# Kernel optimization log

Hardware: AMD Instinct MI355X
Metric: run time of the kernel (lower is better)

Reference implementation:

```python
import jax, jax.numpy as jnp
import numpy as np

N = 16384          # number of vectors to quantize (flattened leading dims)
K = 2 ** 14        # codebook_size = 2**bits_per_codeword
D = 64             # vector_dim


def setup_inputs() -> dict:
    key = jax.random.key(0)
    k1, k2, k3, k4 = jax.random.split(key, 4)
    x_re = jax.random.normal(k1, (N, D), dtype=jnp.float32)
    x_im = jax.random.normal(k2, (N, D), dtype=jnp.float32)
    # random complex codebook, normalized so each row has unit complex L2 norm
    cb_re = jax.random.normal(k3, (K, D), dtype=jnp.float32)
    cb_im = jax.random.normal(k4, (K, D), dtype=jnp.float32)
    norm = jnp.sqrt(jnp.sum(cb_re * cb_re + cb_im * cb_im, axis=1, keepdims=True))
    cb_re = cb_re / norm
    cb_im = cb_im / norm
    return {"x_re": x_re, "x_im": x_im, "cb_re": cb_re, "cb_im": cb_im}


def reference(x_re, x_im, cb_re, cb_im):
    # complex inner product conj(x) . c, expanded in real arithmetic:
    #   Re = x_re.c_re + x_im.c_im ;  Im = x_re.c_im - x_im.c_re
    dot_re = jnp.einsum('nd,kd->nk', x_re, cb_re) + jnp.einsum('nd,kd->nk', x_im, cb_im)
    dot_im = jnp.einsum('nd,kd->nk', x_re, cb_im) - jnp.einsum('nd,kd->nk', x_im, cb_re)
    mag = jnp.sqrt(dot_re * dot_re + dot_im * dot_im)  # [N, K] abs of complex dot
    indices = jnp.argmax(mag, axis=-1)                 # [N] int
    # reconstruction: gather codebook rows (call() with int input)
    recon = jnp.stack([cb_re[indices], cb_im[indices]], axis=-1)  # [N, D, 2] (re, im)
    return indices, recon
```

## Files before the change

kernel.cpp:

```cpp
#include <hip/hip_runtime.h>

#define NROWS 16384
#define KCB   16384
#define DD    64
#define BM    256
#define CSPLIT 16
#define COLS_PER_BLOCK 1024
#define TILE_COLS 128
#define NTILES (COLS_PER_BLOCK / TILE_COLS)
#define NCHUNK (TILE_COLS / 16)
#define CAP 2048
#define DELTA 0.45f
#define TILE_BYTES 32768

typedef __attribute__((ext_vector_type(8))) short bf16x8;
typedef __attribute__((ext_vector_type(4))) float f32x4;

__device__ __forceinline__ unsigned pk_bf16(float lo, float hi) {
    unsigned a = __float_as_uint(lo);
    unsigned b = __float_as_uint(hi);
    a += 0x7FFFu + ((a >> 16) & 1u);
    b += 0x7FFFu + ((b >> 16) & 1u);
    return (a >> 16) | (b & 0xFFFF0000u);
}

__device__ __forceinline__ bf16x8 mk8(unsigned a, unsigned b, unsigned c, unsigned d) {
    union { uint4 u; bf16x8 v; } x;
    x.u = make_uint4(a, b, c, d);
    return x.v;
}

__device__ __forceinline__ unsigned swz(unsigned row, unsigned byte_in_row) {
    return row * 128u + (byte_in_row ^ ((row & 7u) << 4));
}

__device__ __forceinline__ void gload_lds16(const void* g, void* l) {
    __builtin_amdgcn_global_load_lds(
        (__attribute__((address_space(1))) void*)(g),
        (__attribute__((address_space(3))) void*)(l), 16, 0, 0);
}

__global__ __launch_bounds__(256) void prep(
    const float* __restrict__ cb_re, const float* __restrict__ cb_im,
    uint4* __restrict__ cb_sw,
    unsigned* __restrict__ row_max_bits, unsigned long long* __restrict__ best_packed,
    int do_conv)
{
    int id = blockIdx.x * 256 + threadIdx.x;
    if (id < NROWS) { row_max_bits[id] = 0u; best_packed[id] = 0ull; }
    if (!do_conv) return;
    int u   = id & 1023;
    int arr = (id >> 10) & 1;
    int gt  = id >> 11;
    int c   = u >> 3;
    int b   = ((u & 7) * 16) ^ ((c & 7) << 4);
    int col = gt * TILE_COLS + c;
    int d0  = b >> 1;
    const float* src = arr ? cb_im : cb_re;
    const float4* p = (const float4*)(src + (size_t)col * DD + d0);
    float4 f0 = p[0], f1 = p[1];
    cb_sw[id] = make_uint4(pk_bf16(f0.x, f0.y), pk_bf16(f0.z, f0.w),
                           pk_bf16(f1.x, f1.y), pk_bf16(f1.z, f1.w));
}

template<int PASS, bool PRE>
__global__ __launch_bounds__(512, 2) void score_kernel(
    const float* __restrict__ x_re, const float* __restrict__ x_im,
    const float* __restrict__ cb_re, const float* __restrict__ cb_im,
    const char* __restrict__ cb_sw,
    unsigned* __restrict__ row_max_bits,
    unsigned long long* __restrict__ best_packed)
{
    __shared__ char Bls[2][2][TILE_COLS * 128];
    __shared__ unsigned cand[CAP];
    __shared__ int cand_cnt;

    const int tid  = threadIdx.x;
    const int lane = tid & 63;
    const int wid  = tid >> 6;
    const int row0 = blockIdx.x * BM;
    const int col0 = blockIdx.y * COLS_PER_BLOCK;
    const int l15  = lane & 15;
    const int lhi  = lane >> 4;

    if (tid == 0) cand_cnt = 0;

    bf16x8 Ar[2][2], Ai[2][2];
#pragma unroll
    for (int a = 0; a < 2; ++a) {
        const int row = row0 + wid * 32 + a * 16 + l15;
        {
            const float4* pr = (const float4*)(x_re + (size_t)row * DD + lhi * 8);
            const float4* pi = (const float4*)(x_im + (size_t)row * DD + lhi * 8);
            float4 r0 = pr[0], r1 = pr[1];
            float4 i0 = pi[0], i1 = pi[1];
            Ar[a][0] = mk8(pk_bf16(r0.x, r0.y), pk_bf16(r0.z, r0.w),
                           pk_bf16(r1.x, r1.y), pk_bf16(r1.z, r1.w));
            Ai[a][0] = mk8(pk_bf16(i0.x, i0.y), pk_bf16(i0.z, i0.w),
                           pk_bf16(i1.x, i1.y), pk_bf16(i1.z, i1.w));
        }
        {
            const float4* pr = (const float4*)(x_re + (size_t)row * DD + 32 + lhi * 8);
            const float4* pi = (const float4*)(x_im + (size_t)row * DD + 32 + lhi * 8);
            float4 r0 = pr[0], r1 = pr[1];
            float4 i0 = pi[0], i1 = pi[1];
            Ar[a][1] = mk8(pk_bf16(r0.x, r0.y), pk_bf16(r0.z, r0.w),
                           pk_bf16(r1.x, r1.y), pk_bf16(r1.z, r1.w));
            Ai[a][1] = mk8(pk_bf16(i0.x, i0.y), pk_bf16(i0.z, i0.w),
                           pk_bf16(i1.x, i1.y), pk_bf16(i1.z, i1.w));
        }
    }

    float rm[2][4];
    float thr[2][4];
#pragma unroll
    for (int a = 0; a < 2; ++a)
#pragma unroll
        for (int r = 0; r < 4; ++r) rm[a][r] = 0.0f;
    if (PASS == 2) {
#pragma unroll
        for (int a = 0; a < 2; ++a)
#pragma unroll
            for (int r = 0; r < 4; ++r) {
                int n = row0 + wid * 32 + a * 16 + lhi * 4 + r;
                float mx = __uint_as_float(row_max_bits[n]);
                float tm = sqrtf(mx) - DELTA;
                thr[a][r] = (tm > 0.0f) ? tm * tm : -1.0f;
            }
    }

#define CHUNK_BODY(T_IDX, CH)                                                   \
    {                                                                           \
        const char* B0 = &Bls[(T_IDX) & 1][0][0];                               \
        const char* B1 = &Bls[(T_IDX) & 1][1][0];                               \
        const int colLocal = (CH) * 16 + l15;                                   \
        unsigned off0 = swz(colLocal, lhi * 16);                                \
        unsigned off1 = swz(colLocal, 64 + lhi * 16);                           \
        bf16x8 br0 = *(const bf16x8*)(B0 + off0);                               \
        bf16x8 bi0 = *(const bf16x8*)(B1 + off0);                               \
        bf16x8 br1 = *(const bf16x8*)(B0 + off1);                               \
        bf16x8 bi1 = *(const bf16x8*)(B1 + off1);                               \
        f32x4 accre[2], accim[2];                                               \
        _Pragma("unroll")                                                       \
        for (int a = 0; a < 2; ++a) {                                           \
            accre[a] = (f32x4){0.f, 0.f, 0.f, 0.f};                             \
            accim[a] = (f32x4){0.f, 0.f, 0.f, 0.f};                             \
        }                                                                       \
        _Pragma("unroll")                                                       \
        for (int a = 0; a < 2; ++a) {                                           \
            accre[a] = __builtin_amdgcn_mfma_f32_16x16x32_bf16(Ar[a][0], br0, accre[a], 0, 0, 0); \
            accre[a] = __builtin_amdgcn_mfma_f32_16x16x32_bf16(Ai[a][0], bi0, accre[a], 0, 0, 0); \
            accre[a] = __builtin_amdgcn_mfma_f32_16x16x32_bf16(Ar[a][1], br1, accre[a], 0, 0, 0); \
            accre[a] = __builtin_amdgcn_mfma_f32_16x16x32_bf16(Ai[a][1], bi1, accre[a], 0, 0, 0); \
            accim[a] = __builtin_amdgcn_mfma_f32_16x16x32_bf16(Ar[a][0], bi0, accim[a], 0, 0, 0); \
            accim[a] = __builtin_amdgcn_mfma_f32_16x16x32_bf16(Ar[a][1], bi1, accim[a], 0, 0, 0); \
        }                                                                       \
        br0 = br0 ^ (short)0x8000;                                              \
        br1 = br1 ^ (short)0x8000;                                              \
        _Pragma("unroll")                                                       \
        for (int a = 0; a < 2; ++a) {                                           \
            accim[a] = __builtin_amdgcn_mfma_f32_16x16x32_bf16(Ai[a][0], br0, accim[a], 0, 0, 0); \
            accim[a] = __builtin_amdgcn_mfma_f32_16x16x32_bf16(Ai[a][1], br1, accim[a], 0, 0, 0); \
        }                                                                       \
        _Pragma("unroll")                                                       \
        for (int a = 0; a < 2; ++a)                                             \
            _Pragma("unroll")                                                   \
            for (int r = 0; r < 4; ++r) {                                       \
                float re = accre[a][r], im = accim[a][r];                       \
                float m2 = fmaf(re, re, im * im);                               \
                if (PASS == 1) {                                                \
                    rm[a][r] = fmaxf(rm[a][r], m2);                             \
                } else {                                                        \
                    if (m2 >= thr[a][r]) {                                      \
                        int n = row0 + wid * 32 + a * 16 + lhi * 4 + r;         \
                        int k = col0 + (T_IDX) * TILE_COLS + (CH) * 16 + l15;   \
                        int idx = atomicAdd(&cand_cnt, 1);                      \
                        if (idx < CAP) cand[idx] = ((unsigned)n << 14) | (unsigned)k; \
                    }                                                           \
                }                                                               \
            }                                                                   \
    }

    if constexpr (PRE) {
        const char* tile_base = cb_sw + (size_t)blockIdx.y * NTILES * TILE_BYTES;
        auto stage = [&](int buf, int t) {
            const char* src = tile_base + (size_t)t * TILE_BYTES;
            char* dst = &Bls[buf][0][0];
#pragma unroll
            for (int j = 0; j < 4; ++j)
                gload_lds16(src + j * 8192 + tid * 16, dst + j * 8192 + tid * 16);
        };

        stage(0, 0);
        __syncthreads();

        for (int t = 0; t < NTILES; ++t) {
            const int cur = t & 1;
            if (t + 1 < NTILES) {
                stage(cur ^ 1, t + 1);
                asm volatile("s_waitcnt vmcnt(4)" ::: "memory");
            } else {
                asm volatile("s_waitcnt vmcnt(0)" ::: "memory");
            }
            __builtin_amdgcn_sched_barrier(0);
            __builtin_amdgcn_s_barrier();
            __builtin_amdgcn_sched_barrier(0);

            for (int ch = 0; ch < NCHUNK; ++ch)
                CHUNK_BODY(t, ch)

            __builtin_amdgcn_sched_barrier(0);
            __builtin_amdgcn_s_barrier();
        }
        __syncthreads();
    } else {
        const int scol  = tid >> 2;
        const int sboff = (tid & 3) * 32;
        uint4 g[4];
        auto stage_load = [&](int t) {
            const int col = col0 + t * TILE_COLS + scol;
            const int d0  = (tid & 3) * 16;
            const float4* pr = (const float4*)(cb_re + (size_t)col * DD + d0);
            const float4* pi = (const float4*)(cb_im + (size_t)col * DD + d0);
            float4 a0 = pr[0], a1 = pr[1], a2 = pr[2], a3 = pr[3];
            float4 b0 = pi[0], b1 = pi[1], b2 = pi[2], b3 = pi[3];
            g[0] = make_uint4(pk_bf16(a0.x,a0.y), pk_bf16(a0.z,a0.w), pk_bf16(a1.x,a1.y), pk_bf16(a1.z,a1.w));
            g[1] = make_uint4(pk_bf16(a2.x,a2.y), pk_bf16(a2.z,a2.w), pk_bf16(a3.x,a3.y), pk_bf16(a3.z,a3.w));
            g[2] = make_uint4(pk_bf16(b0.x,b0.y), pk_bf16(b0.z,b0.w), pk_bf16(b1.x,b1.y), pk_bf16(b1.z,b1.w));
            g[3] = make_uint4(pk_bf16(b2.x,b2.y), pk_bf16(b2.z,b2.w), pk_bf16(b3.x,b3.y), pk_bf16(b3.z,b3.w));
        };
        auto stage_write = [&](int buf) {
            unsigned o0 = swz(scol, sboff);
            unsigned o1 = swz(scol, sboff + 16);
            *(uint4*)(&Bls[buf][0][0] + o0) = g[0];
            *(uint4*)(&Bls[buf][0][0] + o1) = g[1];
            *(uint4*)(&Bls[buf][1][0] + o0) = g[2];
            *(uint4*)(&Bls[buf][1][0] + o1) = g[3];
        };
        stage_load(0);
        stage_write(0);
        __syncthreads();
        for (int t = 0; t < NTILES; ++t) {
            if (t + 1 < NTILES) stage_load(t + 1);
            for (int ch = 0; ch < NCHUNK; ++ch)
                CHUNK_BODY(t, ch)
            if (t + 1 < NTILES) {
                stage_write(1 - (t & 1));
                __syncthreads();
            }
        }
        __syncthreads();
    }
#undef CHUNK_BODY

    if (PASS == 1) {
#pragma unroll
        for (int m = 1; m < 16; m <<= 1)
#pragma unroll
            for (int a = 0; a < 2; ++a)
#pragma unroll
                for (int r = 0; r < 4; ++r)
                    rm[a][r] = fmaxf(rm[a][r], __shfl_xor(rm[a][r], m, 64));
        if (l15 == 0) {
#pragma unroll
            for (int a = 0; a < 2; ++a)
#pragma unroll
                for (int r = 0; r < 4; ++r) {
                    int n = row0 + wid * 32 + a * 16 + lhi * 4 + r;
                    atomicMax(&row_max_bits[n], __float_as_uint(rm[a][r]));
                }
        }
    } else {
        int cnt = cand_cnt < CAP ? cand_cnt : CAP;
        for (int i = tid; i < cnt; i += 512) {
            unsigned e = cand[i];
            int n = (int)(e >> 14);
            int k = (int)(e & 16383u);
            const float* xr = x_re + (size_t)n * DD;
            const float* xi = x_im + (size_t)n * DD;
            const float* cr = cb_re + (size_t)k * DD;
            const float* ci = cb_im + (size_t)k * DD;
            float accr = 0.0f, acci = 0.0f;
            for (int d = 0; d < DD; ++d) {
                float xrv = xr[d], xiv = xi[d], crv = cr[d], civ = ci[d];
                accr = fmaf(xrv, crv, accr);
                accr = fmaf(xiv, civ, accr);
                acci = fmaf(xrv, civ, acci);
                acci = fmaf(-xiv, crv, acci);
            }
            float m2 = accr * accr + acci * acci;
            unsigned long long key =
                ((unsigned long long)__float_as_uint(m2) << 32) | (unsigned)(~(unsigned)k);
            atomicMax(&best_packed[n], key);
        }
    }
}

__global__ __launch_bounds__(256) void finalize(
    const unsigned long long* __restrict__ best_packed,
    const float* __restrict__ cb_re, const float* __restrict__ cb_im,
    float* __restrict__ out)
{
    const int wave = threadIdx.x >> 6;
    const int lane = threadIdx.x & 63;
    const int n = blockIdx.x * 4 + wave;
    if (n >= NROWS) return;

    unsigned long long p = best_packed[n];
    unsigned k = ~(unsigned)(p & 0xFFFFFFFFull);

    if (lane == 0) out[n] = (float)k;

    float re = cb_re[(size_t)k * DD + lane];
    float im = cb_im[(size_t)k * DD + lane];
    float2* ro = reinterpret_cast<float2*>(out + NROWS);
    ro[(size_t)n * DD + lane] = make_float2(re, im);
}

extern "C" void kernel_launch(void* const* d_in, const int* in_sizes, int n_in,
                              void* d_out, int out_size, void* d_ws, size_t ws_size,
                              hipStream_t stream)
{
    const float* x_re  = (const float*)d_in[0];
    const float* x_im  = (const float*)d_in[1];
    const float* cb_re = (const float*)d_in[2];
    const float* cb_im = (const float*)d_in[3];
    float* out = (float*)d_out;

    const size_t CB_SW_BYTES = (size_t)(KCB / TILE_COLS) * TILE_BYTES;
    const size_t NEED = CB_SW_BYTES + NROWS * 4 + NROWS * 8;
    const bool pre = (ws_size >= NEED);

    const char* cb_sw = (const char*)d_ws;
    unsigned* row_max_bits;
    unsigned long long* best_packed;
    if (pre) {
        row_max_bits = (unsigned*)((char*)d_ws + CB_SW_BYTES);
        best_packed  = (unsigned long long*)((char*)d_ws + CB_SW_BYTES + NROWS * 4);
    } else {
        row_max_bits = (unsigned*)d_ws;
        best_packed  = (unsigned long long*)((char*)d_ws + NROWS * 4);
    }

    prep<<<pre ? 1024 : (NROWS / 256), 256, 0, stream>>>(
        cb_re, cb_im, (uint4*)d_ws, row_max_bits, best_packed, pre ? 1 : 0);

    dim3 grid(NROWS / BM, CSPLIT);
    if (pre) {
        score_kernel<1, true><<<grid, 512, 0, stream>>>(x_re, x_im, cb_re, cb_im,
            cb_sw, row_max_bits, best_packed);
        score_kernel<2, true><<<grid, 512, 0, stream>>>(x_re, x_im, cb_re, cb_im,
            cb_sw, row_max_bits, best_packed);
    } else {
        score_kernel<1, false><<<grid, 512, 0, stream>>>(x_re, x_im, cb_re, cb_im,
            cb_sw, row_max_bits, best_packed);
        score_kernel<2, false><<<grid, 512, 0, stream>>>(x_re, x_im, cb_re, cb_im,
            cb_sw, row_max_bits, best_packed);
    }

    finalize<<<NROWS / 4, 256, 0, stream>>>(best_packed, cb_re, cb_im, out);
}
```

Baseline: 268.7 us.

## Fuse two-pass max/candidate scoring into a single pass with block-local thresholds

Replaces the two score passes (global row max, then candidate emission) with one kernel. Each block tracks per-row maxima in shared memory, starts emitting candidates once the first two tiles have set a threshold, and re-scores tiles 0 and 1 at the end. The column split drops to 8 so each block sees 2048 columns, which gives a tighter local max. Shared-memory overflow now falls back to inline exact rescoring. This removes one full MFMA pass over the codebook. In exchange, block-local thresholds are looser than a global max, so more candidates may be produced, and the non-precomputed fallback path is removed.

Result: slower. 496.6 us (+84.8%).

```diff
diff --git a/kernel.cpp b/kernel.cpp
--- a/kernel.cpp
+++ b/kernel.cpp
@@ -4,12 +4,12 @@
 #define KCB   16384
 #define DD    64
 #define BM    256
-#define CSPLIT 16
-#define COLS_PER_BLOCK 1024
+#define CSPLIT 8
+#define COLS_PER_BLOCK 2048
 #define TILE_COLS 128
-#define NTILES (COLS_PER_BLOCK / TILE_COLS)
-#define NCHUNK (TILE_COLS / 16)
-#define CAP 2048
+#define NTILES 16
+#define NCHUNK 8
+#define CAP 3584
 #define DELTA 0.45f
 #define TILE_BYTES 32768
 
@@ -40,15 +40,42 @@
         (__attribute__((address_space(3))) void*)(l), 16, 0, 0);
 }
 
+__device__ __noinline__ void rescore_one(
+    int n, int k,
+    const float* __restrict__ x_re, const float* __restrict__ x_im,
+    const float* __restrict__ cb_re, const float* __restrict__ cb_im,
+    unsigned long long* __restrict__ best_packed)
+{
+    const float4* xr = (const float4*)(x_re + (size_t)n * DD);
+    const float4* xi = (const float4*)(x_im + (size_t)n * DD);
+    const float4* cr = (const float4*)(cb_re + (size_t)k * DD);
+    const float4* ci = (const float4*)(cb_im + (size_t)k * DD);
+    float accr = 0.0f, acci = 0.0f;
+#pragma unroll 4
+    for (int d4 = 0; d4 < 16; ++d4) {
+        float4 a = xr[d4], b = xi[d4], c = cr[d4], e = ci[d4];
+        accr = fmaf(a.x, c.x, accr); accr = fmaf(b.x, e.x, accr);
+        acci = fmaf(a.x, e.x, acci); acci = fmaf(-b.x, c.x, acci);
+        accr = fmaf(a.y, c.y, accr); accr = fmaf(b.y, e.y, accr);
+        acci = fmaf(a.y, e.y, acci); acci = fmaf(-b.y, c.y, acci);
+        accr = fmaf(a.z, c.z, accr); accr = fmaf(b.z, e.z, accr);
+        acci = fmaf(a.z, e.z, acci); acci = fmaf(-b.z, c.z, acci);
+        accr = fmaf(a.w, c.w, accr); accr = fmaf(b.w, e.w, accr);
+        acci = fmaf(a.w, e.w, acci); acci = fmaf(-b.w, c.w, acci);
+    }
+    float m2 = accr * accr + acci * acci;
+    unsigned long long key =
+        ((unsigned long long)__float_as_uint(m2) << 32) | (unsigned)(~(unsigned)k);
+    atomicMax(best_packed + n, key);
+}
+
 __global__ __launch_bounds__(256) void prep(
     const float* __restrict__ cb_re, const float* __restrict__ cb_im,
     uint4* __restrict__ cb_sw,
-    unsigned* __restrict__ row_max_bits, unsigned long long* __restrict__ best_packed,
-    int do_conv)
+    unsigned long long* __restrict__ best_packed)
 {
     int id = blockIdx.x * 256 + threadIdx.x;
-    if (id < NROWS) { row_max_bits[id] = 0u; best_packed[id] = 0ull; }
-    if (!do_conv) return;
+    if (id < NROWS) best_packed[id] = 0ull;
     int u   = id & 1023;
     int arr = (id >> 10) & 1;
     int gt  = id >> 11;
@@ -63,16 +90,15 @@
                            pk_bf16(f1.x, f1.y), pk_bf16(f1.z, f1.w));
 }
 
-template<int PASS, bool PRE>
 __global__ __launch_bounds__(512, 2) void score_kernel(
     const float* __restrict__ x_re, const float* __restrict__ x_im,
     const float* __restrict__ cb_re, const float* __restrict__ cb_im,
     const char* __restrict__ cb_sw,
-    unsigned* __restrict__ row_max_bits,
     unsigned long long* __restrict__ best_packed)
 {
     __shared__ char Bls[2][2][TILE_COLS * 128];
     __shared__ unsigned cand[CAP];
+    __shared__ unsigned smax[BM];
     __shared__ int cand_cnt;
 
     const int tid  = threadIdx.x;
@@ -84,6 +110,7 @@
     const int lhi  = lane >> 4;
 
     if (tid == 0) cand_cnt = 0;
+    if (tid < BM) smax[tid] = 0u;
 
     bf16x8 Ar[2][2], Ai[2][2];
 #pragma unroll
@@ -116,20 +143,18 @@
 #pragma unroll
     for (int a = 0; a < 2; ++a)
 #pragma unroll
-        for (int r = 0; r < 4; ++r) rm[a][r] = 0.0f;
-    if (PASS == 2) {
+        for (int r = 0; r < 4; ++r) { rm[a][r] = 0.0f; thr[a][r] = __builtin_inff(); }
+
+    const char* tile_base = cb_sw + (size_t)blockIdx.y * NTILES * TILE_BYTES;
+    auto stage = [&](int buf, int t) {
+        const char* src = tile_base + (size_t)t * TILE_BYTES;
+        char* dst = &Bls[buf][0][0];
 #pragma unroll
-        for (int a = 0; a < 2; ++a)
-#pragma unroll
-            for (int r = 0; r < 4; ++r) {
-                int n = row0 + wid * 32 + a * 16 + lhi * 4 + r;
-                float mx = __uint_as_float(row_max_bits[n]);
-                float tm = sqrtf(mx) - DELTA;
-                thr[a][r] = (tm > 0.0f) ? tm * tm : -1.0f;
-            }
-    }
-
-#define CHUNK_BODY(T_IDX, CH)                                                   \
+        for (int j = 0; j < 4; ++j)
+            gload_lds16(src + j * 8192 + tid * 16, dst + j * 8192 + tid * 16);
+    };
+
+#define CHUNK_BODY(T_IDX, CH, TRACK, EMIT)                                      \
     {                                                                           \
         const char* B0 = &Bls[(T_IDX) & 1][0][0];                               \
         const char* B1 = &Bls[(T_IDX) & 1][1][0];                               \
@@ -168,131 +193,101 @@
             for (int r = 0; r < 4; ++r) {                                       \
                 float re = accre[a][r], im = accim[a][r];                       \
                 float m2 = fmaf(re, re, im * im);                               \
-                if (PASS == 1) {                                                \
-                    rm[a][r] = fmaxf(rm[a][r], m2);                             \
-                } else {                                                        \
+                if (TRACK) rm[a][r] = fmaxf(rm[a][r], m2);                      \
+                if (EMIT) {                                                     \
                     if (m2 >= thr[a][r]) {                                      \
-                        int n = row0 + wid * 32 + a * 16 + lhi * 4 + r;         \
-                        int k = col0 + (T_IDX) * TILE_COLS + (CH) * 16 + l15;   \
+                        int nl = wid * 32 + a * 16 + lhi * 4 + r;               \
+                        int k  = col0 + (T_IDX) * TILE_COLS + (CH) * 16 + l15;  \
                         int idx = atomicAdd(&cand_cnt, 1);                      \
-                        if (idx < CAP) cand[idx] = ((unsigned)n << 14) | (unsigned)k; \
+                        if (idx < CAP) {                                        \
+                            cand[idx] = ((unsigned)nl << 14) | (unsigned)k;     \
+                        } else {                                                \
+                               \
+                            rescore_one(row0 + nl, k, x_re, x_im,               \
+                                        cb_re, cb_im, best_packed);             \
+                        }                                                       \
                     }                                                           \
                 }                                                               \
             }                                                                   \
     }
 
-    if constexpr (PRE) {
-        const char* tile_base = cb_sw + (size_t)blockIdx.y * NTILES * TILE_BYTES;
-        auto stage = [&](int buf, int t) {
-            const char* src = tile_base + (size_t)t * TILE_BYTES;
-            char* dst = &Bls[buf][0][0];
-#pragma unroll
-            for (int j = 0; j < 4; ++j)
-                gload_lds16(src + j * 8192 + tid * 16, dst + j * 8192 + tid * 16);
-        };
-
-        stage(0, 0);
-        __syncthreads();
-
-        for (int t = 0; t < NTILES; ++t) {
-            const int cur = t & 1;
-            if (t + 1 < NTILES) {
-                stage(cur ^ 1, t + 1);
-                asm volatile("s_waitcnt vmcnt(4)" ::: "memory");
-            } else {
-                asm volatile("s_waitcnt vmcnt(0)" ::: "memory");
-            }
-            __builtin_amdgcn_sched_barrier(0);
-            __builtin_amdgcn_s_barrier();
-            __builtin_amdgcn_sched_barrier(0);
-
+#define FOLD_SMAX()                                                             \
+    {                                                                           \
+        _Pragma("unroll")                                                       \
+        for (int m = 1; m < 16; m <<= 1)                                        \
+            _Pragma("unroll")                                                   \
+            for (int a = 0; a < 2; ++a)                                         \
+                _Pragma("unroll")                                               \
+                for (int r = 0; r < 4; ++r)                                     \
+                    rm[a][r] = fmaxf(rm[a][r], __shfl_xor(rm[a][r], m, 64));    \
+        if (l15 == 0) {                                                         \
+            _Pragma("unroll")                                                   \
+            for (int a = 0; a < 2; ++a)                                         \
+                _Pragma("unroll")                                               \
+                for (int r = 0; r < 4; ++r)                                     \
+                    atomicMax(&smax[wid * 32 + a * 16 + lhi * 4 + r],           \
+                              __float_as_uint(rm[a][r]));                       \
+        }                                                                       \
+    }
+
+#define LOAD_THR()                                                              \
+    {                                                                           \
+        _Pragma("unroll")                                                       \
+        for (int a = 0; a < 2; ++a)                                             \
+            _Pragma("unroll")                                                   \
+            for (int r = 0; r < 4; ++r) {                                       \
+                float mx = __uint_as_float(smax[wid * 32 + a * 16 + lhi * 4 + r]); \
+                float tm = sqrtf(mx) - DELTA;                                   \
+                thr[a][r] = (tm > 0.0f) ? tm * tm : -1.0f;                      \
+            }                                                                   \
+    }
+
+    stage(0, 0);
+    __syncthreads();
+
+    for (int t = 0; t < NTILES; ++t) {
+        stage((t + 1) & 1, (t + 1) & 15);
+        asm volatile("s_waitcnt vmcnt(4)" ::: "memory");
+        __builtin_amdgcn_sched_barrier(0);
+        __builtin_amdgcn_s_barrier();
+        __builtin_amdgcn_sched_barrier(0);
+
+        if (t >= 2) {
+            LOAD_THR()
             for (int ch = 0; ch < NCHUNK; ++ch)
-                CHUNK_BODY(t, ch)
-
-            __builtin_amdgcn_sched_barrier(0);
-            __builtin_amdgcn_s_barrier();
+                CHUNK_BODY(t, ch, 1, 1)
+        } else {
+            for (int ch = 0; ch < NCHUNK; ++ch)
+                CHUNK_BODY(t, ch, 1, 0)
         }
-        __syncthreads();
-    } else {
-        const int scol  = tid >> 2;
-        const int sboff = (tid & 3) * 32;
-        uint4 g[4];
-        auto stage_load = [&](int t) {
-            const int col = col0 + t * TILE_COLS + scol;
-            const int d0  = (tid & 3) * 16;
-            const float4* pr = (const float4*)(cb_re + (size_t)col * DD + d0);
-            const float4* pi = (const float4*)(cb_im + (size_t)col * DD + d0);
-            float4 a0 = pr[0], a1 = pr[1], a2 = pr[2], a3 = pr[3];
-            float4 b0 = pi[0], b1 = pi[1], b2 = pi[2], b3 = pi[3];
-            g[0] = make_uint4(pk_bf16(a0.x,a0.y), pk_bf16(a0.z,a0.w), pk_bf16(a1.x,a1.y), pk_bf16(a1.z,a1.w));
-            g[1] = make_uint4(pk_bf16(a2.x,a2.y), pk_bf16(a2.z,a2.w), pk_bf16(a3.x,a3.y), pk_bf16(a3.z,a3.w));
-            g[2] = make_uint4(pk_bf16(b0.x,b0.y), pk_bf16(b0.z,b0.w), pk_bf16(b1.x,b1.y), pk_bf16(b1.z,b1.w));
-            g[3] = make_uint4(pk_bf16(b2.x,b2.y), pk_bf16(b2.z,b2.w), pk_bf16(b3.x,b3.y), pk_bf16(b3.z,b3.w));
-        };
-        auto stage_write = [&](int buf) {
-            unsigned o0 = swz(scol, sboff);
-            unsigned o1 = swz(scol, sboff + 16);
-            *(uint4*)(&Bls[buf][0][0] + o0) = g[0];
-            *(uint4*)(&Bls[buf][0][0] + o1) = g[1];
-            *(uint4*)(&Bls[buf][1][0] + o0) = g[2];
-            *(uint4*)(&Bls[buf][1][0] + o1) = g[3];
-        };
-        stage_load(0);
-        stage_write(0);
-        __syncthreads();
-        for (int t = 0; t < NTILES; ++t) {
-            if (t + 1 < NTILES) stage_load(t + 1);
-            for (int ch = 0; ch < NCHUNK; ++ch)
-                CHUNK_BODY(t, ch)
-            if (t + 1 < NTILES) {
-                stage_write(1 - (t & 1));
-                __syncthreads();
-            }
-        }
-        __syncthreads();
-    }
+        FOLD_SMAX()
+
+        __builtin_amdgcn_sched_barrier(0);
+        __builtin_amdgcn_s_barrier();
+    }
+
+    stage(1, 1);
+    asm volatile("s_waitcnt vmcnt(0)" ::: "memory");
+    __builtin_amdgcn_sched_barrier(0);
+    __builtin_amdgcn_s_barrier();
+    __builtin_amdgcn_sched_barrier(0);
+    LOAD_THR()
+    for (int ch = 0; ch < NCHUNK; ++ch)
+        CHUNK_BODY(0, ch, 0, 1)
+    for (int ch = 0; ch < NCHUNK; ++ch)
+        CHUNK_BODY(1, ch, 0, 1)
+
+    __syncthreads();
+
 #undef CHUNK_BODY
-
-    if (PASS == 1) {
-#pragma unroll
-        for (int m = 1; m < 16; m <<= 1)
-#pragma unroll
-            for (int a = 0; a < 2; ++a)
-#pragma unroll
-                for (int r = 0; r < 4; ++r)
-                    rm[a][r] = fmaxf(rm[a][r], __shfl_xor(rm[a][r], m, 64));
-        if (l15 == 0) {
-#pragma unroll
-            for (int a = 0; a < 2; ++a)
-#pragma unroll
-                for (int r = 0; r < 4; ++r) {
-                    int n = row0 + wid * 32 + a * 16 + lhi * 4 + r;
-                    atomicMax(&row_max_bits[n], __float_as_uint(rm[a][r]));
-                }
-        }
-    } else {
-        int cnt = cand_cnt < CAP ? cand_cnt : CAP;
-        for (int i = tid; i < cnt; i += 512) {
-            unsigned e = cand[i];
-            int n = (int)(e >> 14);
-            int k = (int)(e & 16383u);
-            const float* xr = x_re + (size_t)n * DD;
-            const float* xi = x_im + (size_t)n * DD;
-            const float* cr = cb_re + (size_t)k * DD;
-            const float* ci = cb_im + (size_t)k * DD;
-            float accr = 0.0f, acci = 0.0f;
-            for (int d = 0; d < DD; ++d) {
-                float xrv = xr[d], xiv = xi[d], crv = cr[d], civ = ci[d];
-                accr = fmaf(xrv, crv, accr);
-                accr = fmaf(xiv, civ, accr);
-                acci = fmaf(xrv, civ, acci);
-                acci = fmaf(-xiv, crv, acci);
-            }
-            float m2 = accr * accr + acci * acci;
-            unsigned long long key =
-                ((unsigned long long)__float_as_uint(m2) << 32) | (unsigned)(~(unsigned)k);
-            atomicMax(&best_packed[n], key);
-        }
+#undef FOLD_SMAX
+#undef LOAD_THR
+
+    int cnt = cand_cnt < CAP ? cand_cnt : CAP;
+    for (int i = tid; i < cnt; i += 512) {
+        unsigned e = cand[i];
+        rescore_one(row0 + (int)(e >> 14), (int)(e & 16383u),
+                    x_re, x_im, cb_re, cb_im, best_packed);
     }
 }
 
@@ -328,35 +323,15 @@
     float* out = (float*)d_out;
 
     const size_t CB_SW_BYTES = (size_t)(KCB / TILE_COLS) * TILE_BYTES;
-    const size_t NEED = CB_SW_BYTES + NROWS * 4 + NROWS * 8;
-    const bool pre = (ws_size >= NEED);
-
-    const char* cb_sw = (const char*)d_ws;
-    unsigned* row_max_bits;
-    unsigned long long* best_packed;
-    if (pre) {
-        row_max_bits = (unsigned*)((char*)d_ws + CB_SW_BYTES);
-        best_packed  = (unsigned long long*)((char*)d_ws + CB_SW_BYTES + NROWS * 4);
-    } else {
-        row_max_bits = (unsigned*)d_ws;
-        best_packed  = (unsigned long long*)((char*)d_ws + NROWS * 4);
-    }
-
-    prep<<<pre ? 1024 : (NROWS / 256), 256, 0, stream>>>(
-        cb_re, cb_im, (uint4*)d_ws, row_max_bits, best_packed, pre ? 1 : 0);
+    char* p = (char*)d_ws;
+    const char* cb_sw = p;                                        p += CB_SW_BYTES;
+    unsigned long long* best_packed = (unsigned long long*)p;
+
+    prep<<<1024, 256, 0, stream>>>(cb_re, cb_im, (uint4*)d_ws, best_packed);
 
     dim3 grid(NROWS / BM, CSPLIT);
-    if (pre) {
-        score_kernel<1, true><<<grid, 512, 0, stream>>>(x_re, x_im, cb_re, cb_im,
-            cb_sw, row_max_bits, best_packed);
-        score_kernel<2, true><<<grid, 512, 0, stream>>>(x_re, x_im, cb_re, cb_im,
-            cb_sw, row_max_bits, best_packed);
-    } else {
-        score_kernel<1, false><<<grid, 512, 0, stream>>>(x_re, x_im, cb_re, cb_im,
-            cb_sw, row_max_bits, best_packed);
-        score_kernel<2, false><<<grid, 512, 0, stream>>>(x_re, x_im, cb_re, cb_im,
-            cb_sw, row_max_bits, best_packed);
-    }
+    score_kernel<<<grid, 512, 0, stream>>>(x_re, x_im, cb_re, cb_im,
+                                           cb_sw, best_packed);
 
     finalize<<<NROWS / 4, 256, 0, stream>>>(best_packed, cb_re, cb_im, out);
 }
```
